# Kernel optimization log

Hardware: AMD Instinct MI355X
Metric: run time of the kernel (lower is better)

The kernel has to match this reference:

```python
import jax, jax.numpy as jnp
import numpy as np

N_NODES = 100000
N_EDGES = 1600000
IN_DIM = 128
FEAT_DIM = 128
N_CLS = 40


def _glorot(key, shape):
    fan_in = shape[1]
    bound = 1.0 / np.sqrt(fan_in)
    return jax.random.uniform(key, shape, jnp.float32, -bound, bound)


def setup_inputs() -> dict:
    key = jax.random.key(0)
    ks = jax.random.split(key, 12)
    x = jax.random.normal(ks[0], (N_NODES, IN_DIM), jnp.float32)
    edge_index = jax.random.randint(ks[1], (2, N_EDGES), 0, N_NODES, jnp.int64)
    edge_weight = jax.random.uniform(ks[2], (N_EDGES,), jnp.float32)
    # layer 1 (in=IN_DIM, out=FEAT_DIM)
    W1_l = _glorot(ks[3], (FEAT_DIM, IN_DIM))
    b1_l = jnp.zeros((FEAT_DIM,), jnp.float32)
    W1_r = _glorot(ks[4], (FEAT_DIM, IN_DIM))
    # layer 2 (in=FEAT_DIM, out=FEAT_DIM)
    W2_l = _glorot(ks[5], (FEAT_DIM, FEAT_DIM))
    b2_l = jnp.zeros((FEAT_DIM,), jnp.float32)
    W2_r = _glorot(ks[6], (FEAT_DIM, FEAT_DIM))
    # classifier
    Wc = _glorot(ks[7], (N_CLS, FEAT_DIM))
    bc = jnp.zeros((N_CLS,), jnp.float32)
    return {"x": x, "edge_index": edge_index, "edge_weight": edge_weight,
            "W1_l": W1_l, "b1_l": b1_l, "W1_r": W1_r,
            "W2_l": W2_l, "b2_l": b2_l, "W2_r": W2_r,
            "Wc": Wc, "bc": bc}


def _sage_conv(x, src, dst, W_l, b_l, W_r):
    # mean aggregation of neighbor features: mean_{j in N(i)} x_j
    msg = x[src]                                        # [E, F] gather
    agg = jax.ops.segment_sum(msg, dst, num_segments=N_NODES)  # [N, F]
    deg = jax.ops.segment_sum(jnp.ones((src.shape[0],), x.dtype), dst,
                              num_segments=N_NODES)     # [N]
    mean = agg / jnp.maximum(deg, 1.0)[:, None]         # isolated nodes -> 0
    out = mean @ W_l.T + b_l                            # lin_l
    out = out + x @ W_r.T                               # root (temp_weight)
    return out


def reference(x, edge_index, edge_weight, W1_l, b1_l, W1_r, W2_l, b2_l, W2_r, Wc, bc):
    src = edge_index[0]
    dst = edge_index[1]
    h = jax.nn.relu(_sage_conv(x, src, dst, W1_l, b1_l, W1_r))
    h = jax.nn.relu(_sage_conv(h, src, dst, W2_l, b2_l, W2_r))
    # dropout is identity in eval mode
    return h @ Wc.T + bc
```

## Files before the change

kernel.cpp:

```cpp
#include <hip/hip_runtime.h>

#define NN 100000
#define NE 1600000
#define FD 128
#define NC 40
#define NBK 782
#define HISTB 256
#define CONVB 512
#define CHUNK (NE / HISTB)

typedef __attribute__((ext_vector_type(8))) short short8;
typedef __attribute__((ext_vector_type(4))) float f32x4;

#define WS_OFF      0u
#define WS_INVDEG   400384u
#define WS_CNT      800512u
#define WS_BTOT     1601280u
#define WS_BKO      1604480u
#define WS_WB       1607680u
#define WS_CSR      1880576u
#define WS_XB       8280576u
#define WS_MB       33880576u
#define WS_HB       59480576u

__device__ inline unsigned short bf16_rne(float v) {
    union { float f; unsigned u; } a; a.f = v;
    return (unsigned short)((a.u + 0x7FFFu + ((a.u >> 16) & 1u)) >> 16);
}

__device__ inline void cvt_split(float v, unsigned short& h, unsigned short& l) {
    union { float f; unsigned u; } a; a.f = v;
    unsigned rh = (a.u + 0x7FFFu + ((a.u >> 16) & 1u)) >> 16;
    h = (unsigned short)rh;
    union { unsigned u; float f; } b; b.u = rh << 16;
    float lo = v - b.f;
    union { float f; unsigned u; } c; c.f = lo;
    l = (unsigned short)((c.u + 0x7FFFu + ((c.u >> 16) & 1u)) >> 16);
}

__global__ __launch_bounds__(256) void k_p1(
        const int* __restrict__ ei, int* __restrict__ cnt,
        const float* __restrict__ x, unsigned short* __restrict__ xb) {
    if (blockIdx.x < CONVB) {
        int i = blockIdx.x * 256 + threadIdx.x;
        const int total = NN * FD / 8;
        for (int s = i; s < total; s += CONVB * 256) {
            float4 a = *reinterpret_cast<const float4*>(x + (size_t)s * 8);
            float4 b = *reinterpret_cast<const float4*>(x + (size_t)s * 8 + 4);
            short8 o;
            o[0] = (short)bf16_rne(a.x); o[1] = (short)bf16_rne(a.y);
            o[2] = (short)bf16_rne(a.z); o[3] = (short)bf16_rne(a.w);
            o[4] = (short)bf16_rne(b.x); o[5] = (short)bf16_rne(b.y);
            o[6] = (short)bf16_rne(b.z); o[7] = (short)bf16_rne(b.w);
            *reinterpret_cast<short8*>(xb + (size_t)s * 8) = o;
        }
    } else {
        __shared__ int hist[NBK];
        const int* dst = ei + NE;
        int blk = blockIdx.x - CONVB;
        for (int j = threadIdx.x; j < NBK; j += 256) hist[j] = 0;
        __syncthreads();
        int base = blk * CHUNK;
        for (int i = threadIdx.x; i < CHUNK; i += 256)
            atomicAdd(&hist[dst[base + i] >> 7], 1);
        __syncthreads();
        for (int j = threadIdx.x; j < NBK; j += 256)
            cnt[blk * NBK + j] = hist[j];
    }
}

__global__ __launch_bounds__(256) void k_p2a(int* __restrict__ cnt,
                                             int* __restrict__ btot) {
    __shared__ int s[256];
    int b = blockIdx.x, t = threadIdx.x;
    int v = cnt[t * NBK + b];
    s[t] = v;
    __syncthreads();
    for (int d = 1; d < 256; d <<= 1) {
        int x = (t >= d) ? s[t - d] : 0;
        __syncthreads();
        s[t] += x;
        __syncthreads();
    }
    cnt[t * NBK + b] = s[t] - v;
    if (t == 255) btot[b] = s[255];
}

__global__ __launch_bounds__(256) void k_p2b(const int* __restrict__ btot,
                                             int* __restrict__ bko) {
    __shared__ int s[256];
    int t = threadIdx.x;
    int base = t * 4;
    int v[4]; int tsum = 0;
#pragma unroll
    for (int j = 0; j < 4; ++j) {
        int idx = base + j;
        v[j] = (idx < NBK) ? btot[idx] : 0;
        tsum += v[j];
    }
    s[t] = tsum;
    __syncthreads();
    for (int d = 1; d < 256; d <<= 1) {
        int x = (t >= d) ? s[t - d] : 0;
        __syncthreads();
        s[t] += x;
        __syncthreads();
    }
    int p = s[t] - tsum;
#pragma unroll
    for (int j = 0; j < 4; ++j) {
        int idx = base + j;
        if (idx <= NBK) bko[idx] = p;
        p += v[j];
    }
}

__global__ __launch_bounds__(256) void k_p3(const int* __restrict__ ei,
                                            const int* __restrict__ cnt,
                                            const int* __restrict__ bko,
                                            unsigned* __restrict__ bval) {
    __shared__ int cur[NBK];
    int blk = blockIdx.x;
    for (int j = threadIdx.x; j < NBK; j += 256)
        cur[j] = bko[j] + cnt[blk * NBK + j];
    __syncthreads();
    int base = blk * CHUNK;
    const int* src = ei;
    const int* dst = ei + NE;
    for (int i = threadIdx.x; i < CHUNK; i += 256) {
        int sv = src[base + i];
        int d  = dst[base + i];
        int pos = atomicAdd(&cur[d >> 7], 1);
        bval[pos] = (unsigned)sv | ((unsigned)(d & 127) << 17);
    }
}

__global__ __launch_bounds__(256) void k_p4(const unsigned* __restrict__ bval,
                                            const int* __restrict__ bko,
                                            int* __restrict__ csr,
                                            int* __restrict__ off,
                                            float* __restrict__ invdeg) {
    __shared__ int hist[128], curk[128], sc[128];
    int b = blockIdx.x, tid = threadIdx.x;
    int s = bko[b], e = bko[b + 1];
    if (tid < 128) hist[tid] = 0;
    __syncthreads();
    for (int i = s + tid; i < e; i += 256)
        atomicAdd(&hist[bval[i] >> 17], 1);
    __syncthreads();
    if (tid < 128) sc[tid] = hist[tid];
    __syncthreads();
    for (int d = 1; d < 128; d <<= 1) {
        int x = (tid >= d && tid < 128) ? sc[tid - d] : 0;
        __syncthreads();
        if (tid < 128) sc[tid] += x;
        __syncthreads();
    }
    if (tid < 128) {
        int excl = sc[tid] - hist[tid];
        curk[tid] = excl;
        int node = b * 128 + tid;
        if (node < NN) {
            off[node] = s + excl;
            int dg = hist[tid];
            invdeg[node] = 1.0f / (float)(dg > 0 ? dg : 1);
        }
    }
    if (b == 0 && tid == 0) off[NN] = NE;
    __syncthreads();
    for (int i = s + tid; i < e; i += 256) {
        unsigned v = bval[i];
        int dl = v >> 17;
        int r = atomicAdd(&curk[dl], 1);
        csr[s + r] = (int)(v & 0x1FFFFu);
    }
}

__global__ void k_prepw(const float* __restrict__ W1l, const float* __restrict__ W1r,
                        const float* __restrict__ W2l, const float* __restrict__ W2r,
                        const float* __restrict__ Wc, unsigned short* __restrict__ wb) {
    int i = blockIdx.x * 256 + threadIdx.x;
    if (i < 65536) {
        int m = i >> 14, e = i & 16383;
        const float* W = (m == 0) ? W1l : (m == 1) ? W1r : (m == 2) ? W2l : W2r;
        unsigned short h, l;
        cvt_split(W[e], h, l);
        wb[m * 32768 + e] = h;
        wb[m * 32768 + 16384 + e] = l;
    } else if (i < 65536 + NC * FD) {
        int j = i - 65536;
        wb[131072 + j] = bf16_rne(Wc[j]);
    }
}

__device__ inline void acc8(float* a, uint4 v) {
    a[0] += __uint_as_float(v.x << 16);
    a[1] += __uint_as_float(v.x & 0xFFFF0000u);
    a[2] += __uint_as_float(v.y << 16);
    a[3] += __uint_as_float(v.y & 0xFFFF0000u);
    a[4] += __uint_as_float(v.z << 16);
    a[5] += __uint_as_float(v.z & 0xFFFF0000u);
    a[6] += __uint_as_float(v.w << 16);
    a[7] += __uint_as_float(v.w & 0xFFFF0000u);
}

__global__ __launch_bounds__(256) void k_agg(const unsigned short* __restrict__ Xb,
                                             const int* __restrict__ off,
                                             const int* __restrict__ csr,
                                             const float* __restrict__ invdeg,
                                             unsigned short* __restrict__ Mb) {
    int wid = (blockIdx.x * 256 + threadIdx.x) >> 6;
    int lane = threadIdx.x & 63;
    if (wid >= NN) return;
    const int g  = lane >> 4;
    const int fc = lane & 15;
    const unsigned short* Xl = Xb + fc * 8;
    int s0 = off[wid], s1 = off[wid + 1];
    float a[8] = {};
    int e = s0;
    for (; e + 7 < s1; e += 8) {
        int r0 = csr[e + g];
        int r1 = csr[e + 4 + g];
        uint4 v0 = *reinterpret_cast<const uint4*>(Xl + ((size_t)r0 << 7));
        uint4 v1 = *reinterpret_cast<const uint4*>(Xl + ((size_t)r1 << 7));
        acc8(a, v0);
        acc8(a, v1);
    }
    for (; e < s1; e += 4) {
        int cnt = s1 - e;
        int r = csr[e + (g < cnt ? g : 0)];
        uint4 v = *reinterpret_cast<const uint4*>(Xl + ((size_t)r << 7));
        if (g < cnt) acc8(a, v);
    }
#pragma unroll
    for (int j = 0; j < 8; ++j) {
        a[j] += __shfl_xor(a[j], 32);
        a[j] += __shfl_xor(a[j], 16);
    }
    if (g == 0) {
        float w = invdeg[wid];
        uint4 o;
        o.x = (unsigned)bf16_rne(a[0] * w) | ((unsigned)bf16_rne(a[1] * w) << 16);
        o.y = (unsigned)bf16_rne(a[2] * w) | ((unsigned)bf16_rne(a[3] * w) << 16);
        o.z = (unsigned)bf16_rne(a[4] * w) | ((unsigned)bf16_rne(a[5] * w) << 16);
        o.w = (unsigned)bf16_rne(a[6] * w) | ((unsigned)bf16_rne(a[7] * w) << 16);
        *reinterpret_cast<uint4*>(Mb + (size_t)wid * FD + fc * 8) = o;
    }
}

template <bool FUSE>
__global__ __launch_bounds__(256, 3) void k_gemm(
        const unsigned short* __restrict__ M,
        const unsigned short* __restrict__ X,
        const unsigned short* __restrict__ Wl,
        const unsigned short* __restrict__ Wr,
        const float* __restrict__ bias,
        const unsigned short* __restrict__ Wcb,
        const float* __restrict__ bc,
        unsigned short* outb, float* outf) {
    __shared__ __align__(16) unsigned short pool[FUSE ? 21504 : 12800];
    unsigned short* Ah = pool;
    unsigned short* Bh = pool + 2560;
    unsigned short* Bl = pool + 7680;

    const int tid = threadIdx.x;
    const int wave = tid >> 6;
    const int lane = tid & 63;
    const int wm = wave & 1;
    const int wn = wave >> 1;
    const int nb = blockIdx.x * 64;
    const int l15 = lane & 15;
    const int kb = lane >> 4;

    f32x4 acc[2][4] = {};

    for (int c = 0; c < 8; ++c) {
        const unsigned short* A = (c < 4) ? M : X;
        const unsigned short* W = (c < 4) ? Wl : Wr;
        const int kc = (c & 3) * 32;
        __syncthreads();
        {
            int row = tid >> 2, seg = tid & 3;
            int gn = nb + row;
            short8 v = {};
            if (gn < NN)
                v = *reinterpret_cast<const short8*>(A + (size_t)gn * FD + kc + seg * 8);
            *reinterpret_cast<short8*>(&Ah[row * 40 + seg * 8]) = v;
        }
#pragma unroll
        for (int r = 0; r < 2; ++r) {
            int slot = tid + 256 * r;
            int o = slot >> 2, seg = slot & 3;
            short8 vh = *reinterpret_cast<const short8*>(W + o * FD + kc + seg * 8);
            short8 vl = *reinterpret_cast<const short8*>(W + 16384 + o * FD + kc + seg * 8);
            *reinterpret_cast<short8*>(&Bh[o * 40 + seg * 8]) = vh;
            *reinterpret_cast<short8*>(&Bl[o * 40 + seg * 8]) = vl;
        }
        __syncthreads();
        short8 a[2], b_h[4], b_l[4];
#pragma unroll
        for (int mt = 0; mt < 2; ++mt) {
            int row = wm * 32 + mt * 16 + l15;
            a[mt] = *reinterpret_cast<const short8*>(&Ah[row * 40 + kb * 8]);
        }
#pragma unroll
        for (int nt = 0; nt < 4; ++nt) {
            int o = wn * 64 + nt * 16 + l15;
            b_h[nt] = *reinterpret_cast<const short8*>(&Bh[o * 40 + kb * 8]);
            b_l[nt] = *reinterpret_cast<const short8*>(&Bl[o * 40 + kb * 8]);
        }
#pragma unroll
        for (int mt = 0; mt < 2; ++mt)
#pragma unroll
            for (int nt = 0; nt < 4; ++nt) {
                acc[mt][nt] = __builtin_amdgcn_mfma_f32_16x16x32_bf16(a[mt], b_h[nt], acc[mt][nt], 0, 0, 0);
                acc[mt][nt] = __builtin_amdgcn_mfma_f32_16x16x32_bf16(a[mt], b_l[nt], acc[mt][nt], 0, 0, 0);
            }
    }

    float bz[4];
#pragma unroll
    for (int nt = 0; nt < 4; ++nt) bz[nt] = bias[wn * 64 + nt * 16 + l15];

    if (!FUSE) {
#pragma unroll
        for (int mt = 0; mt < 2; ++mt) {
            int gn0 = nb + wm * 32 + mt * 16 + kb * 4;
#pragma unroll
            for (int r = 0; r < 4; ++r) {
                int gn = gn0 + r;
                if (gn < NN) {
#pragma unroll
                    for (int nt = 0; nt < 4; ++nt) {
                        float v = fmaxf(acc[mt][nt][r] + bz[nt], 0.f);
                        outb[(size_t)gn * FD + wn * 64 + nt * 16 + l15] = bf16_rne(v);
                    }
                }
            }
        }
    } else {
        unsigned short* Hs  = pool + 12800;
        unsigned short* Wcs = pool;
        __syncthreads();
#pragma unroll
        for (int r = 0; r < 3; ++r) {
            int slot = tid + 256 * r;
            if (slot < 640) {
                int row = slot >> 4, seg = slot & 15;
                *reinterpret_cast<short8*>(&Wcs[row * 136 + seg * 8]) =
                    *reinterpret_cast<const short8*>(Wcb + row * FD + seg * 8);
            }
        }
#pragma unroll
        for (int mt = 0; mt < 2; ++mt) {
            int row0 = wm * 32 + mt * 16 + kb * 4;
#pragma unroll
            for (int r = 0; r < 4; ++r) {
#pragma unroll
                for (int nt = 0; nt < 4; ++nt) {
                    float v = fmaxf(acc[mt][nt][r] + bz[nt], 0.f);
                    Hs[(row0 + r) * 136 + wn * 64 + nt * 16 + l15] = bf16_rne(v);
                }
            }
        }
        __syncthreads();
        f32x4 c2[3] = {};
#pragma unroll
        for (int kk = 0; kk < 4; ++kk) {
            short8 af = *reinterpret_cast<const short8*>(
                &Hs[(wave * 16 + l15) * 136 + kk * 32 + kb * 8]);
#pragma unroll
            for (int t = 0; t < 3; ++t) {
                short8 bf = *reinterpret_cast<const short8*>(
                    &Wcs[(t * 16 + l15) * 136 + kk * 32 + kb * 8]);
                c2[t] = __builtin_amdgcn_mfma_f32_16x16x32_bf16(af, bf, c2[t], 0, 0, 0);
            }
        }
#pragma unroll
        for (int t = 0; t < 3; ++t) {
            int cls = t * 16 + l15;
            if (cls < NC) {
#pragma unroll
                for (int r = 0; r < 4; ++r) {
                    int gn = nb + wave * 16 + kb * 4 + r;
                    if (gn < NN)
                        outf[(size_t)gn * NC + cls] = c2[t][r] + bc[cls];
                }
            }
        }
    }
}

extern "C" void kernel_launch(void* const* d_in, const int* in_sizes, int n_in,
                              void* d_out, int out_size, void* d_ws, size_t ws_size,
                              hipStream_t stream) {
    const float* x   = (const float*)d_in[0];
    const int*   ei  = (const int*)d_in[1];
    const float* W1l = (const float*)d_in[3];
    const float* b1l = (const float*)d_in[4];
    const float* W1r = (const float*)d_in[5];
    const float* W2l = (const float*)d_in[6];
    const float* b2l = (const float*)d_in[7];
    const float* W2r = (const float*)d_in[8];
    const float* Wc  = (const float*)d_in[9];
    const float* bc  = (const float*)d_in[10];
    float* out = (float*)d_out;

    char* ws = (char*)d_ws;
    int*   off    = (int*)(ws + WS_OFF);
    float* invdeg = (float*)(ws + WS_INVDEG);
    int*   cnt    = (int*)(ws + WS_CNT);
    int*   btot   = (int*)(ws + WS_BTOT);
    int*   bko    = (int*)(ws + WS_BKO);
    unsigned short* wb = (unsigned short*)(ws + WS_WB);
    int*   csr    = (int*)(ws + WS_CSR);
    unsigned short* xb = (unsigned short*)(ws + WS_XB);
    unsigned short* mb = (unsigned short*)(ws + WS_MB);
    unsigned short* hb = (unsigned short*)(ws + WS_HB);
    unsigned* bval = (unsigned*)(ws + WS_HB);

    k_prepw<<<276, 256, 0, stream>>>(W1l, W1r, W2l, W2r, Wc, wb);
    k_p1<<<CONVB + HISTB, 256, 0, stream>>>(ei, cnt, x, xb);
    k_p2a<<<NBK, 256, 0, stream>>>(cnt, btot);
    k_p2b<<<1, 256, 0, stream>>>(btot, bko);
    k_p3<<<HISTB, 256, 0, stream>>>(ei, cnt, bko, bval);
    k_p4<<<NBK, 256, 0, stream>>>(bval, bko, csr, off, invdeg);

    const int GG = (NN + 63) / 64;

    k_agg<<<(NN + 3) / 4, 256, 0, stream>>>(xb, off, csr, invdeg, mb);
    k_gemm<false><<<GG, 256, 0, stream>>>(mb, xb, wb, wb + 32768, b1l,
                                          nullptr, nullptr, hb, nullptr);
    k_agg<<<(NN + 3) / 4, 256, 0, stream>>>(hb, off, csr, invdeg, mb);
    k_gemm<true><<<GG, 256, 0, stream>>>(mb, hb, wb + 65536, wb + 98304, b2l,
                                         wb + 131072, bc, nullptr, out);
}
```

Measured before the change: 243.8 us.

## Fuse neighbor mean aggregation into the SAGE GEMM kernel via shared memory

Removes the standalone aggregation kernel. Each GEMM block now gathers and averages neighbor features for its 64 rows and writes the bf16 result straight into an LDS tile, with one wave handling 16 rows. The root features are loaded into the same tile halfway through the K loop. This avoids writing and re-reading the intermediate mean matrix in global memory and saves two launches. In exchange, far fewer waves are available to hide the latency of the irregular gathers, and each block does its aggregation serially before any MFMA work starts.

```diff
diff --git a/kernel.cpp b/kernel.cpp
--- a/kernel.cpp
+++ b/kernel.cpp
@@ -20,8 +20,7 @@
 #define WS_WB       1607680u
 #define WS_CSR      1880576u
 #define WS_XB       8280576u
-#define WS_MB       33880576u
-#define WS_HB       59480576u
+#define WS_HB       33880576u
 
 __device__ inline unsigned short bf16_rne(float v) {
     union { float f; unsigned u; } a; a.f = v;
@@ -204,64 +203,22 @@
     a[7] += __uint_as_float(v.w & 0xFFFF0000u);
 }
 
-__global__ __launch_bounds__(256) void k_agg(const unsigned short* __restrict__ Xb,
-                                             const int* __restrict__ off,
-                                             const int* __restrict__ csr,
-                                             const float* __restrict__ invdeg,
-                                             unsigned short* __restrict__ Mb) {
-    int wid = (blockIdx.x * 256 + threadIdx.x) >> 6;
-    int lane = threadIdx.x & 63;
-    if (wid >= NN) return;
-    const int g  = lane >> 4;
-    const int fc = lane & 15;
-    const unsigned short* Xl = Xb + fc * 8;
-    int s0 = off[wid], s1 = off[wid + 1];
-    float a[8] = {};
-    int e = s0;
-    for (; e + 7 < s1; e += 8) {
-        int r0 = csr[e + g];
-        int r1 = csr[e + 4 + g];
-        uint4 v0 = *reinterpret_cast<const uint4*>(Xl + ((size_t)r0 << 7));
-        uint4 v1 = *reinterpret_cast<const uint4*>(Xl + ((size_t)r1 << 7));
-        acc8(a, v0);
-        acc8(a, v1);
-    }
-    for (; e < s1; e += 4) {
-        int cnt = s1 - e;
-        int r = csr[e + (g < cnt ? g : 0)];
-        uint4 v = *reinterpret_cast<const uint4*>(Xl + ((size_t)r << 7));
-        if (g < cnt) acc8(a, v);
-    }
-#pragma unroll
-    for (int j = 0; j < 8; ++j) {
-        a[j] += __shfl_xor(a[j], 32);
-        a[j] += __shfl_xor(a[j], 16);
-    }
-    if (g == 0) {
-        float w = invdeg[wid];
-        uint4 o;
-        o.x = (unsigned)bf16_rne(a[0] * w) | ((unsigned)bf16_rne(a[1] * w) << 16);
-        o.y = (unsigned)bf16_rne(a[2] * w) | ((unsigned)bf16_rne(a[3] * w) << 16);
-        o.z = (unsigned)bf16_rne(a[4] * w) | ((unsigned)bf16_rne(a[5] * w) << 16);
-        o.w = (unsigned)bf16_rne(a[6] * w) | ((unsigned)bf16_rne(a[7] * w) << 16);
-        *reinterpret_cast<uint4*>(Mb + (size_t)wid * FD + fc * 8) = o;
-    }
-}
-
 template <bool FUSE>
-__global__ __launch_bounds__(256, 3) void k_gemm(
-        const unsigned short* __restrict__ M,
-        const unsigned short* __restrict__ X,
+__global__ __launch_bounds__(256, 4) void k_fused(
+        const unsigned short* __restrict__ Xsrc,
+        const int* __restrict__ off,
+        const int* __restrict__ csr,
+        const float* __restrict__ invdeg,
         const unsigned short* __restrict__ Wl,
         const unsigned short* __restrict__ Wr,
         const float* __restrict__ bias,
         const unsigned short* __restrict__ Wcb,
         const float* __restrict__ bc,
         unsigned short* outb, float* outf) {
-    __shared__ __align__(16) unsigned short pool[FUSE ? 21504 : 12800];
-    unsigned short* Ah = pool;
-    unsigned short* Bh = pool + 2560;
-    unsigned short* Bl = pool + 7680;
+    __shared__ __align__(16) unsigned short pool[18944];
+    unsigned short* Am = pool;
+    unsigned short* Bh = pool + 8704;
+    unsigned short* Bl = pool + 13824;
 
     const int tid = threadIdx.x;
     const int wave = tid >> 6;
@@ -272,20 +229,66 @@
     const int l15 = lane & 15;
     const int kb = lane >> 4;
 
+    {
+        const int g  = lane >> 4;
+        const int fc = lane & 15;
+        const unsigned short* Xl = Xsrc + fc * 8;
+        for (int i = 0; i < 16; ++i) {
+            int row = wave * 16 + i;
+            int wid = nb + row;
+            float a[8] = {};
+            if (wid < NN) {
+                int s0 = off[wid], s1 = off[wid + 1];
+                int e = s0;
+                for (; e + 7 < s1; e += 8) {
+                    int r0 = csr[e + g];
+                    int r1 = csr[e + 4 + g];
+                    uint4 v0 = *reinterpret_cast<const uint4*>(Xl + ((size_t)r0 << 7));
+                    uint4 v1 = *reinterpret_cast<const uint4*>(Xl + ((size_t)r1 << 7));
+                    acc8(a, v0);
+                    acc8(a, v1);
+                }
+                for (; e < s1; e += 4) {
+                    int cntv = s1 - e;
+                    int r = csr[e + (g < cntv ? g : 0)];
+                    uint4 v = *reinterpret_cast<const uint4*>(Xl + ((size_t)r << 7));
+                    if (g < cntv) acc8(a, v);
+                }
+            }
+#pragma unroll
+            for (int j = 0; j < 8; ++j) {
+                a[j] += __shfl_xor(a[j], 32);
+                a[j] += __shfl_xor(a[j], 16);
+            }
+            if (g == 0) {
+                float w = (wid < NN) ? invdeg[wid] : 0.f;
+                short8 o;
+                o[0] = (short)bf16_rne(a[0] * w); o[1] = (short)bf16_rne(a[1] * w);
+                o[2] = (short)bf16_rne(a[2] * w); o[3] = (short)bf16_rne(a[3] * w);
+                o[4] = (short)bf16_rne(a[4] * w); o[5] = (short)bf16_rne(a[5] * w);
+                o[6] = (short)bf16_rne(a[6] * w); o[7] = (short)bf16_rne(a[7] * w);
+                *reinterpret_cast<short8*>(&Am[row * 136 + fc * 8]) = o;
+            }
+        }
+    }
+    __syncthreads();
+
     f32x4 acc[2][4] = {};
-
     for (int c = 0; c < 8; ++c) {
-        const unsigned short* A = (c < 4) ? M : X;
         const unsigned short* W = (c < 4) ? Wl : Wr;
         const int kc = (c & 3) * 32;
-        __syncthreads();
-        {
-            int row = tid >> 2, seg = tid & 3;
-            int gn = nb + row;
-            short8 v = {};
-            if (gn < NN)
-                v = *reinterpret_cast<const short8*>(A + (size_t)gn * FD + kc + seg * 8);
-            *reinterpret_cast<short8*>(&Ah[row * 40 + seg * 8]) = v;
+        if (c) __syncthreads();
+        if (c == 4) {
+#pragma unroll
+            for (int r = 0; r < 4; ++r) {
+                int slot = tid + 256 * r;
+                int row = slot >> 4, seg = slot & 15;
+                int gn = nb + row;
+                short8 v = {};
+                if (gn < NN)
+                    v = *reinterpret_cast<const short8*>(Xsrc + (size_t)gn * FD + seg * 8);
+                *reinterpret_cast<short8*>(&Am[row * 136 + seg * 8]) = v;
+            }
         }
 #pragma unroll
         for (int r = 0; r < 2; ++r) {
@@ -301,7 +304,7 @@
 #pragma unroll
         for (int mt = 0; mt < 2; ++mt) {
             int row = wm * 32 + mt * 16 + l15;
-            a[mt] = *reinterpret_cast<const short8*>(&Ah[row * 40 + kb * 8]);
+            a[mt] = *reinterpret_cast<const short8*>(&Am[row * 136 + kc + kb * 8]);
         }
 #pragma unroll
         for (int nt = 0; nt < 4; ++nt) {
@@ -339,8 +342,8 @@
             }
         }
     } else {
-        unsigned short* Hs  = pool + 12800;
-        unsigned short* Wcs = pool;
+        unsigned short* Hs  = pool;
+        unsigned short* Wcs = pool + 8704;
         __syncthreads();
 #pragma unroll
         for (int r = 0; r < 3; ++r) {
@@ -415,7 +418,6 @@
     unsigned short* wb = (unsigned short*)(ws + WS_WB);
     int*   csr    = (int*)(ws + WS_CSR);
     unsigned short* xb = (unsigned short*)(ws + WS_XB);
-    unsigned short* mb = (unsigned short*)(ws + WS_MB);
     unsigned short* hb = (unsigned short*)(ws + WS_HB);
     unsigned* bval = (unsigned*)(ws + WS_HB);
 
@@ -428,10 +430,10 @@
 
     const int GG = (NN + 63) / 64;
 
-    k_agg<<<(NN + 3) / 4, 256, 0, stream>>>(xb, off, csr, invdeg, mb);
-    k_gemm<false><<<GG, 256, 0, stream>>>(mb, xb, wb, wb + 32768, b1l,
-                                          nullptr, nullptr, hb, nullptr);
-    k_agg<<<(NN + 3) / 4, 256, 0, stream>>>(hb, off, csr, invdeg, mb);
-    k_gemm<true><<<GG, 256, 0, stream>>>(mb, hb, wb + 65536, wb + 98304, b2l,
-                                         wb + 131072, bc, nullptr, out);
-}
+    k_fused<false><<<GG, 256, 0, stream>>>(xb, off, csr, invdeg,
+                                           wb, wb + 32768, b1l,
+                                           nullptr, nullptr, hb, nullptr);
+    k_fused<true><<<GG, 256, 0, stream>>>(hb, off, csr, invdeg,
+                                          wb + 65536, wb + 98304, b2l,
+                                          wb + 131072, bc, nullptr, out);
+}
```

Measured after the change: 302.7 us. 1.24x slower.

## Fuse weight prep into k_p1 and software-pipeline the neighbor gather in k_agg

Applied to the files above, without the earlier changes.

The weight-conversion kernel is folded into the first preprocessing kernel as extra blocks, which removes one kernel launch and lets that work run alongside the x conversion and histogram. The aggregation kernel gains a 16-edge-per-iteration main loop that issues the next group's gathers before accumulating the previous group. This keeps more memory loads in flight per wave and should hide gather latency, at the cost of higher register pressure.

```diff
diff --git a/kernel.cpp b/kernel.cpp
--- a/kernel.cpp
+++ b/kernel.cpp
@@ -7,6 +7,7 @@
 #define NBK 782
 #define HISTB 256
 #define CONVB 512
+#define PREPB 276
 #define CHUNK (NE / HISTB)
 
 typedef __attribute__((ext_vector_type(8))) short short8;
@@ -40,7 +41,10 @@
 
 __global__ __launch_bounds__(256) void k_p1(
         const int* __restrict__ ei, int* __restrict__ cnt,
-        const float* __restrict__ x, unsigned short* __restrict__ xb) {
+        const float* __restrict__ x, unsigned short* __restrict__ xb,
+        const float* __restrict__ W1l, const float* __restrict__ W1r,
+        const float* __restrict__ W2l, const float* __restrict__ W2r,
+        const float* __restrict__ Wc, unsigned short* __restrict__ wb) {
     if (blockIdx.x < CONVB) {
         int i = blockIdx.x * 256 + threadIdx.x;
         const int total = NN * FD / 8;
@@ -54,7 +58,7 @@
             o[6] = (short)bf16_rne(b.z); o[7] = (short)bf16_rne(b.w);
             *reinterpret_cast<short8*>(xb + (size_t)s * 8) = o;
         }
-    } else {
+    } else if (blockIdx.x < CONVB + HISTB) {
         __shared__ int hist[NBK];
         const int* dst = ei + NE;
         int blk = blockIdx.x - CONVB;
@@ -66,6 +70,19 @@
         __syncthreads();
         for (int j = threadIdx.x; j < NBK; j += 256)
             cnt[blk * NBK + j] = hist[j];
+    } else {
+        int i = (blockIdx.x - CONVB - HISTB) * 256 + threadIdx.x;
+        if (i < 65536) {
+            int m = i >> 14, e = i & 16383;
+            const float* W = (m == 0) ? W1l : (m == 1) ? W1r : (m == 2) ? W2l : W2r;
+            unsigned short h, l;
+            cvt_split(W[e], h, l);
+            wb[m * 32768 + e] = h;
+            wb[m * 32768 + 16384 + e] = l;
+        } else if (i < 65536 + NC * FD) {
+            int j = i - 65536;
+            wb[131072 + j] = bf16_rne(Wc[j]);
+        }
     }
 }
 
@@ -173,23 +190,6 @@
         int dl = v >> 17;
         int r = atomicAdd(&curk[dl], 1);
         csr[s + r] = (int)(v & 0x1FFFFu);
-    }
-}
-
-__global__ void k_prepw(const float* __restrict__ W1l, const float* __restrict__ W1r,
-                        const float* __restrict__ W2l, const float* __restrict__ W2r,
-                        const float* __restrict__ Wc, unsigned short* __restrict__ wb) {
-    int i = blockIdx.x * 256 + threadIdx.x;
-    if (i < 65536) {
-        int m = i >> 14, e = i & 16383;
-        const float* W = (m == 0) ? W1l : (m == 1) ? W1r : (m == 2) ? W2l : W2r;
-        unsigned short h, l;
-        cvt_split(W[e], h, l);
-        wb[m * 32768 + e] = h;
-        wb[m * 32768 + 16384 + e] = l;
-    } else if (i < 65536 + NC * FD) {
-        int j = i - 65536;
-        wb[131072 + j] = bf16_rne(Wc[j]);
     }
 }
 
@@ -218,6 +218,25 @@
     int s0 = off[wid], s1 = off[wid + 1];
     float a[8] = {};
     int e = s0;
+    if (e + 15 < s1) {
+        uint4 p0 = *reinterpret_cast<const uint4*>(Xl + ((size_t)csr[e + g]      << 7));
+        uint4 p1 = *reinterpret_cast<const uint4*>(Xl + ((size_t)csr[e + 4 + g]  << 7));
+        uint4 p2 = *reinterpret_cast<const uint4*>(Xl + ((size_t)csr[e + 8 + g]  << 7));
+        uint4 p3 = *reinterpret_cast<const uint4*>(Xl + ((size_t)csr[e + 12 + g] << 7));
+        for (e += 16; e + 15 < s1; e += 16) {
+            int j0 = csr[e + g];
+            int j1 = csr[e + 4 + g];
+            int j2 = csr[e + 8 + g];
+            int j3 = csr[e + 12 + g];
+            uint4 n0 = *reinterpret_cast<const uint4*>(Xl + ((size_t)j0 << 7));
+            uint4 n1 = *reinterpret_cast<const uint4*>(Xl + ((size_t)j1 << 7));
+            uint4 n2 = *reinterpret_cast<const uint4*>(Xl + ((size_t)j2 << 7));
+            uint4 n3 = *reinterpret_cast<const uint4*>(Xl + ((size_t)j3 << 7));
+            acc8(a, p0); acc8(a, p1); acc8(a, p2); acc8(a, p3);
+            p0 = n0; p1 = n1; p2 = n2; p3 = n3;
+        }
+        acc8(a, p0); acc8(a, p1); acc8(a, p2); acc8(a, p3);
+    }
     for (; e + 7 < s1; e += 8) {
         int r0 = csr[e + g];
         int r1 = csr[e + 4 + g];
@@ -419,8 +438,8 @@
     unsigned short* hb = (unsigned short*)(ws + WS_HB);
     unsigned* bval = (unsigned*)(ws + WS_HB);
 
-    k_prepw<<<276, 256, 0, stream>>>(W1l, W1r, W2l, W2r, Wc, wb);
-    k_p1<<<CONVB + HISTB, 256, 0, stream>>>(ei, cnt, x, xb);
+    k_p1<<<CONVB + HISTB + PREPB, 256, 0, stream>>>(ei, cnt, x, xb,
+                                                    W1l, W1r, W2l, W2r, Wc, wb);
     k_p2a<<<NBK, 256, 0, stream>>>(cnt, btot);
     k_p2b<<<1, 256, 0, stream>>>(btot, bko);
     k_p3<<<HISTB, 256, 0, stream>>>(ei, cnt, bko, bval);
```

New measurement: 235.2 us. -3.5%, faster.
